# Kernel optimization log

Hardware: AMD Instinct MI355X
Metric: run time of the kernel (lower is better)

## Reference

```python
import jax, jax.numpy as jnp
import numpy as np

N, S, R, CM = 1, 128, 256, 256
C, CZ = 32, 128


def setup_inputs() -> dict:
    key = jax.random.key(0)
    k1, k2, k3, k4 = jax.random.split(key, 4)
    return {
        "msa_repr": jax.random.normal(k1, (N, S, R, CM), dtype=jnp.float32),
        "left_proj": jax.random.normal(k2, (CM, C), dtype=jnp.float32) * 0.05,
        "right_proj": jax.random.normal(k3, (CM, C), dtype=jnp.float32) * 0.05,
        "out_proj": jax.random.normal(k4, (C * C, CZ), dtype=jnp.float32) * 0.05,
    }


def reference(msa_repr, left_proj, right_proj, out_proj):
    # msa_repr: [N, S, R, CM]
    # Project to left/right activations and move R before S
    # (equivalent to torch matmul + transpose(-2, -3)).
    a = jnp.einsum("nsrm,mc->nrsc", msa_repr, left_proj)   # [N, R, S, C]
    b = jnp.einsum("nsrm,mc->nrsc", msa_repr, right_proj)  # [N, R, S, C]
    # Outer product contracted over the MSA dim S:
    # outer[n, r, t, c, e] = sum_s a[n, r, s, c] * b[n, t, s, e]
    outer = jnp.einsum("nrsc,ntse->nrtce", a, b)            # [N, R, R, C, C]
    n, r, t = outer.shape[:3]
    outer = outer.reshape(n, r, t, C * C)                   # [N, R, R, C*C]
    # Output projection to pair channels cz
    return outer @ out_proj                                 # [N, R, R, CZ]
```

## Files before the change

kernel.cpp:

```cpp
#include <hip/hip_runtime.h>

typedef __bf16 bf16x8 __attribute__((ext_vector_type(8)));
typedef __bf16 bf16x4 __attribute__((ext_vector_type(4)));
typedef float f32x16 __attribute__((ext_vector_type(16)));
typedef float f32x4 __attribute__((ext_vector_type(4)));

constexpr int S = 128, R = 256, CM = 256, C = 32, CZ = 128;

#define MFMA __builtin_amdgcn_mfma_f32_32x32x16_bf16

__device__ __forceinline__ bf16x4 cvt4(float a, float b, float c, float d) {
    bf16x4 r;
    r[0] = (__bf16)a; r[1] = (__bf16)b; r[2] = (__bf16)c; r[3] = (__bf16)d;
    return r;
}

__global__ __launch_bounds__(256) void k_wt(const float* __restrict__ W,
                                            __bf16* __restrict__ WTf) {
    int g = blockIdx.x * 256 + threadIdx.x;
    int cz = g & 127;
    int k = g >> 7;
    int e = k >> 5, c = k & 31;
    float v = W[(size_t)(c * 32 + e) * 128 + cz];
    WTf[((size_t)(k >> 3) * 128 + cz) * 8 + (k & 7)] = (__bf16)v;
}

__global__ __launch_bounds__(256) void k_wlr(const float* __restrict__ Lp,
                                             const float* __restrict__ Rp,
                                             __bf16* __restrict__ WLRT) {
    int c = blockIdx.x;
    int m = threadIdx.x;
    const float* src = (c < 32) ? Lp : Rp;
    WLRT[(size_t)c * 256 + m] = (__bf16)src[(size_t)m * 32 + (c & 31)];
}

__global__ __launch_bounds__(512) void k_proj(const float* __restrict__ msa,
                                              const __bf16* __restrict__ WLRT,
                                              __bf16* __restrict__ aTf,
                                              __bf16* __restrict__ bTf) {
    __shared__ __align__(16) __bf16 As[64 * 256];
    __shared__ __align__(16) char Pp[4 * 4096];
    const int r = blockIdx.x;
    const int sh = blockIdx.y;
    const int t = threadIdx.x;

#pragma unroll
    for (int it = 0; it < 8; ++it) {
        int idx = it * 512 + t;
        int row = idx >> 6;
        int cg = idx & 63;
        float4 v = *(const float4*)&msa[((size_t)(sh * 64 + row) * R + r) * CM + cg * 4];
        bf16x4 h = cvt4(v.x, v.y, v.z, v.w);
        int P = (cg >> 1) ^ (row & 15);
        *(bf16x4*)((char*)As + row * 512 + P * 16 + (cg & 1) * 8) = h;
    }
    __syncthreads();

    const int w = t >> 6;
    const int l = t & 63;
    const int l31 = t & 31;
    const int kh = (t >> 5) & 1;
    const int ksh = w >> 2;
    const int sd = (w >> 1) & 1;
    const int mi = w & 1;

    f32x16 acc;
#pragma unroll
    for (int q = 0; q < 16; ++q) acc[q] = 0.f;

    const bf16x8* wb = (const bf16x8*)&WLRT[(size_t)(sd * 32 + l31) * 256 + 8 * kh];
    const int srow = mi * 32 + l31;
    const char* arow = (const char*)As + srow * 512;

    __builtin_amdgcn_s_setprio(1);
#pragma unroll
    for (int j = 0; j < 8; ++j) {
        int ks = ksh * 8 + j;
        int P = (2 * ks + kh) ^ (srow & 15);
        bf16x8 af = *(const bf16x8*)(arow + P * 16);
        acc = MFMA(af, wb[2 * ks], acc, 0, 0, 0);
    }
    __builtin_amdgcn_s_setprio(0);

    char* pbase = Pp + (size_t)(sd * 2 + mi) * 4096;
    if (ksh == 1) {
#pragma unroll
        for (int pc = 0; pc < 4; ++pc) {
            f32x4 v;
            v[0] = acc[4 * pc + 0]; v[1] = acc[4 * pc + 1];
            v[2] = acc[4 * pc + 2]; v[3] = acc[4 * pc + 3];
            *(f32x4*)(pbase + ((pc * 64) + l) * 16) = v;
        }
    }
    __syncthreads();
    if (ksh == 0) {
#pragma unroll
        for (int pc = 0; pc < 4; ++pc) {
            f32x4 v = *(const f32x4*)(pbase + ((pc * 64) + l) * 16);
            acc[4 * pc + 0] += v[0]; acc[4 * pc + 1] += v[1];
            acc[4 * pc + 2] += v[2]; acc[4 * pc + 3] += v[3];
        }
        __bf16* dst = sd ? bTf : aTf;
        const int wg = sh * 2 + mi;
#pragma unroll
        for (int q = 0; q < 4; ++q) {
            size_t base = (size_t)r * 4096 + (size_t)(2 * wg + (q >> 1)) * 512 +
                          (size_t)(q & 1) * 256 + (size_t)l31 * 8 + 4 * kh;
            *(bf16x4*)&dst[base] = cvt4(acc[4 * q + 0], acc[4 * q + 1],
                                        acc[4 * q + 2], acc[4 * q + 3]);
        }
    }
}

__global__ __launch_bounds__(1024, 4) void k_main(const __bf16* __restrict__ aTf,
                                                  const __bf16* __restrict__ bTf,
                                                  const __bf16* __restrict__ WTf,
                                                  float* __restrict__ out) {
    __shared__ __align__(16) __bf16 Gs[64 * 1024];

    const int t = threadIdx.x;
    const int w = t >> 6;
    const int l = t & 63;
    const int lane = l & 31;
    const int kh = l >> 5;
    const int r0 = blockIdx.x * 8;
    const int t0 = blockIdx.y * 8;

    const int rg = w >> 2;
    const int tg = w & 3;

    f32x16 acc[2][2];
#pragma unroll
    for (int i = 0; i < 2; ++i)
#pragma unroll
        for (int j = 0; j < 2; ++j)
#pragma unroll
            for (int q = 0; q < 16; ++q) acc[i][j][q] = 0.f;

    const bf16x8* ap0 = (const bf16x8*)aTf + ((size_t)(r0 + 2 * rg + 0) * 512 + kh * 32 + lane);
    const bf16x8* ap1 = (const bf16x8*)aTf + ((size_t)(r0 + 2 * rg + 1) * 512 + kh * 32 + lane);
    const bf16x8* bp0 = (const bf16x8*)bTf + ((size_t)(t0 + 2 * tg + 0) * 512 + kh * 32 + lane);
    const bf16x8* bp1 = (const bf16x8*)bTf + ((size_t)(t0 + 2 * tg + 1) * 512 + kh * 32 + lane);

    bf16x8 A0[2], B0[2], A1[2], B1[2];
#define LDA(Aa, Bb, ks) do { \
    Aa[0] = ap0[(ks) * 64]; Aa[1] = ap1[(ks) * 64]; \
    Bb[0] = bp0[(ks) * 64]; Bb[1] = bp1[(ks) * 64]; } while (0)
#define PH_A(Aa, Bb) do { \
    __builtin_amdgcn_s_setprio(1); \
    acc[0][0] = MFMA(Aa[0], Bb[0], acc[0][0], 0, 0, 0); \
    acc[0][1] = MFMA(Aa[0], Bb[1], acc[0][1], 0, 0, 0); \
    acc[1][0] = MFMA(Aa[1], Bb[0], acc[1][0], 0, 0, 0); \
    acc[1][1] = MFMA(Aa[1], Bb[1], acc[1][1], 0, 0, 0); \
    __builtin_amdgcn_s_setprio(0); } while (0)

    LDA(A0, B0, 0);
#pragma unroll
    for (int ks = 0; ks < 8; ks += 2) {
        LDA(A1, B1, ks + 1);
        PH_A(A0, B0);
        LDA(A0, B0, (ks + 2) & 7);
        PH_A(A1, B1);
    }

#pragma unroll
    for (int i = 0; i < 2; ++i) {
#pragma unroll
        for (int j = 0; j < 2; ++j) {
            int p = (2 * rg + i) * 8 + 2 * tg + j;
            unsigned prow = (unsigned)p * 2048;
#pragma unroll
            for (int q = 0; q < 4; ++q) {
                int Lc = lane * 4 + q;
                int P = Lc ^ (p & 15) ^ (lane & 7);
                *(bf16x4*)((char*)Gs + prow + (unsigned)P * 16 + kh * 8) =
                    cvt4(acc[i][j][4 * q + 0], acc[i][j][4 * q + 1],
                         acc[i][j][4 * q + 2], acc[i][j][4 * q + 3]);
            }
        }
    }
    __syncthreads();

    const int kq = w >> 2;
    const int mt = (w >> 1) & 1;
    const int ng = w & 1;
    const int czl0 = ng * 64 + lane;
    const int czl1 = czl0 + 32;
    const bf16x8* wb0 = (const bf16x8*)WTf + ((size_t)kh * 128 + czl0);
    const bf16x8* wb1 = (const bf16x8*)WTf + ((size_t)kh * 128 + czl1);
    const unsigned prowG = (unsigned)(mt * 32 + lane) * 2048;
    const int p15 = lane & 15;

    f32x16 o0, o1;
#pragma unroll
    for (int q = 0; q < 16; ++q) { o0[q] = 0.f; o1[q] = 0.f; }

    bf16x8 Wa0, Wa1, Ga, Wb0_, Wb1_, Gb;
#define LDB(W0v, W1v, Gv, kk) do { \
    W0v = wb0[(size_t)(kk) * 256]; \
    W1v = wb1[(size_t)(kk) * 256]; \
    int Lr = (kk) * 2 + kh; \
    int P = Lr ^ p15 ^ ((Lr >> 2) & 7); \
    Gv = *(const bf16x8*)((const char*)Gs + prowG + (unsigned)P * 16); } while (0)
#define PHB(W0v, W1v, Gv) do { \
    __builtin_amdgcn_s_setprio(1); \
    o0 = MFMA(Gv, W0v, o0, 0, 0, 0); \
    o1 = MFMA(Gv, W1v, o1, 0, 0, 0); \
    __builtin_amdgcn_s_setprio(0); } while (0)

    LDB(Wa0, Wa1, Ga, kq * 16);
#pragma unroll
    for (int j = 0; j < 16; j += 2) {
        LDB(Wb0_, Wb1_, Gb, kq * 16 + ((j + 1) & 15));
        PHB(Wa0, Wa1, Ga);
        LDB(Wa0, Wa1, Ga, kq * 16 + ((j + 2) & 15));
        PHB(Wb0_, Wb1_, Gb);
    }
    __syncthreads();

    if (kq > 0) {
        char* pr = (char*)Gs + (size_t)((kq - 1) * 4 + mt * 2 + ng) * 8192;
#pragma unroll
        for (int oi = 0; oi < 2; ++oi) {
            const f32x16& ov = oi ? o1 : o0;
#pragma unroll
            for (int pc = 0; pc < 4; ++pc) {
                f32x4 v;
                v[0] = ov[4 * pc + 0]; v[1] = ov[4 * pc + 1];
                v[2] = ov[4 * pc + 2]; v[3] = ov[4 * pc + 3];
                *(f32x4*)(pr + ((oi * 4 + pc) * 64 + l) * 16) = v;
            }
        }
    }
    __syncthreads();

    if (kq == 0) {
#pragma unroll
        for (int kq2 = 1; kq2 < 4; ++kq2) {
            const char* pr = (const char*)Gs + (size_t)((kq2 - 1) * 4 + mt * 2 + ng) * 8192;
#pragma unroll
            for (int pc = 0; pc < 4; ++pc) {
                f32x4 v0 = *(const f32x4*)(pr + ((pc) * 64 + l) * 16);
                f32x4 v1 = *(const f32x4*)(pr + ((4 + pc) * 64 + l) * 16);
                o0[4 * pc + 0] += v0[0]; o0[4 * pc + 1] += v0[1];
                o0[4 * pc + 2] += v0[2]; o0[4 * pc + 3] += v0[3];
                o1[4 * pc + 0] += v1[0]; o1[4 * pc + 1] += v1[1];
                o1[4 * pc + 2] += v1[2]; o1[4 * pc + 3] += v1[3];
            }
        }
#pragma unroll
        for (int reg = 0; reg < 16; ++reg) {
            int pl = mt * 32 + (reg & 3) + 8 * (reg >> 2) + 4 * kh;
            int pr2 = pl >> 3, pt = pl & 7;
            out[((size_t)(r0 + pr2) * 256 + (t0 + pt)) * 128 + czl0] = o0[reg];
            out[((size_t)(r0 + pr2) * 256 + (t0 + pt)) * 128 + czl1] = o1[reg];
        }
    }
}

extern "C" void kernel_launch(void* const* d_in, const int* in_sizes, int n_in,
                              void* d_out, int out_size, void* d_ws, size_t ws_size,
                              hipStream_t stream) {
    const float* msa = (const float*)d_in[0];
    const float* left = (const float*)d_in[1];
    const float* right = (const float*)d_in[2];
    const float* W = (const float*)d_in[3];

    __bf16* aTf = (__bf16*)d_ws;
    __bf16* bTf = aTf + (size_t)R * 4096;
    __bf16* WTf = bTf + (size_t)R * 4096;
    __bf16* WLRT = WTf + (size_t)128 * 1024;
    float* outp = (float*)d_out;

    k_wt<<<512, 256, 0, stream>>>(W, WTf);
    k_wlr<<<64, 256, 0, stream>>>(left, right, WLRT);
    k_proj<<<dim3(256, 2), 512, 0, stream>>>(msa, WLRT, aTf, bTf);
    k_main<<<dim3(32, 32), 1024, 0, stream>>>(aTf, bTf, WTf, outp);
}
```

Before: 66.95 us.

## Stage a/b tiles in LDS, remap output-projection waves, merge prep kernels

The two weight-preparation kernels are merged into a single launch, removing one kernel launch. In k_main the block's 8 rows of a and 8 rows of b are first loaded cooperatively into LDS and then read from there for the outer-product MFMAs. Previously each wave fetched them from global memory directly, with redundant loads across waves. The output-projection stage is remapped so each wave loads one W fragment and reuses it for two G row tiles, halving W global loads per wave. The cost is an extra LDS staging pass and additional barriers.

```diff
diff --git a/kernel.cpp b/kernel.cpp
--- a/kernel.cpp
+++ b/kernel.cpp
@@ -15,23 +15,25 @@
     return r;
 }
 
-__global__ __launch_bounds__(256) void k_wt(const float* __restrict__ W,
-                                            __bf16* __restrict__ WTf) {
-    int g = blockIdx.x * 256 + threadIdx.x;
-    int cz = g & 127;
-    int k = g >> 7;
-    int e = k >> 5, c = k & 31;
-    float v = W[(size_t)(c * 32 + e) * 128 + cz];
-    WTf[((size_t)(k >> 3) * 128 + cz) * 8 + (k & 7)] = (__bf16)v;
-}
-
-__global__ __launch_bounds__(256) void k_wlr(const float* __restrict__ Lp,
-                                             const float* __restrict__ Rp,
-                                             __bf16* __restrict__ WLRT) {
-    int c = blockIdx.x;
-    int m = threadIdx.x;
-    const float* src = (c < 32) ? Lp : Rp;
-    WLRT[(size_t)c * 256 + m] = (__bf16)src[(size_t)m * 32 + (c & 31)];
+__global__ __launch_bounds__(256) void k_prep(const float* __restrict__ W,
+                                              const float* __restrict__ Lp,
+                                              const float* __restrict__ Rp,
+                                              __bf16* __restrict__ WTf,
+                                              __bf16* __restrict__ WLRT) {
+    int b = blockIdx.x;
+    if (b < 512) {
+        int g = b * 256 + threadIdx.x;
+        int cz = g & 127;
+        int k = g >> 7;
+        int e = k >> 5, c = k & 31;
+        float v = W[(size_t)(c * 32 + e) * 128 + cz];
+        WTf[((size_t)(k >> 3) * 128 + cz) * 8 + (k & 7)] = (__bf16)v;
+    } else {
+        int c = b - 512;
+        int m = threadIdx.x;
+        const float* src = (c < 32) ? Lp : Rp;
+        WLRT[(size_t)c * 256 + m] = (__bf16)src[(size_t)m * 32 + (c & 31)];
+    }
 }
 
 __global__ __launch_bounds__(512) void k_proj(const float* __restrict__ msa,
@@ -116,7 +118,7 @@
                                                   const __bf16* __restrict__ bTf,
                                                   const __bf16* __restrict__ WTf,
                                                   float* __restrict__ out) {
-    __shared__ __align__(16) __bf16 Gs[64 * 1024];
+    __shared__ __align__(16) __bf16 Lds[64 * 1024];
 
     const int t = threadIdx.x;
     const int w = t >> 6;
@@ -126,6 +128,26 @@
     const int r0 = blockIdx.x * 8;
     const int t0 = blockIdx.y * 8;
 
+    {
+        const bf16x8* ga = (const bf16x8*)(aTf + (size_t)r0 * 4096);
+        const bf16x8* gb = (const bf16x8*)(bTf + (size_t)t0 * 4096);
+        bf16x8* ls = (bf16x8*)Lds;
+        bf16x8 va[4], vb[4];
+#pragma unroll
+        for (int i = 0; i < 4; ++i) {
+            int idx = i * 1024 + t;
+            va[i] = ga[idx];
+            vb[i] = gb[idx];
+        }
+#pragma unroll
+        for (int i = 0; i < 4; ++i) {
+            int idx = i * 1024 + t;
+            ls[idx] = va[i];
+            ls[4096 + idx] = vb[i];
+        }
+    }
+    __syncthreads();
+
     const int rg = w >> 2;
     const int tg = w & 3;
 
@@ -137,15 +159,17 @@
 #pragma unroll
             for (int q = 0; q < 16; ++q) acc[i][j][q] = 0.f;
 
-    const bf16x8* ap0 = (const bf16x8*)aTf + ((size_t)(r0 + 2 * rg + 0) * 512 + kh * 32 + lane);
-    const bf16x8* ap1 = (const bf16x8*)aTf + ((size_t)(r0 + 2 * rg + 1) * 512 + kh * 32 + lane);
-    const bf16x8* bp0 = (const bf16x8*)bTf + ((size_t)(t0 + 2 * tg + 0) * 512 + kh * 32 + lane);
-    const bf16x8* bp1 = (const bf16x8*)bTf + ((size_t)(t0 + 2 * tg + 1) * 512 + kh * 32 + lane);
+    const char* a0p = (const char*)Lds + (2 * rg + 0) * 8192 + kh * 512 + lane * 16;
+    const char* a1p = (const char*)Lds + (2 * rg + 1) * 8192 + kh * 512 + lane * 16;
+    const char* b0p = (const char*)Lds + 65536 + (2 * tg + 0) * 8192 + kh * 512 + lane * 16;
+    const char* b1p = (const char*)Lds + 65536 + (2 * tg + 1) * 8192 + kh * 512 + lane * 16;
 
     bf16x8 A0[2], B0[2], A1[2], B1[2];
 #define LDA(Aa, Bb, ks) do { \
-    Aa[0] = ap0[(ks) * 64]; Aa[1] = ap1[(ks) * 64]; \
-    Bb[0] = bp0[(ks) * 64]; Bb[1] = bp1[(ks) * 64]; } while (0)
+    Aa[0] = *(const bf16x8*)(a0p + (ks) * 1024); \
+    Aa[1] = *(const bf16x8*)(a1p + (ks) * 1024); \
+    Bb[0] = *(const bf16x8*)(b0p + (ks) * 1024); \
+    Bb[1] = *(const bf16x8*)(b1p + (ks) * 1024); } while (0)
 #define PH_A(Aa, Bb) do { \
     __builtin_amdgcn_s_setprio(1); \
     acc[0][0] = MFMA(Aa[0], Bb[0], acc[0][0], 0, 0, 0); \
@@ -162,6 +186,7 @@
         LDA(A0, B0, (ks + 2) & 7);
         PH_A(A1, B1);
     }
+    __syncthreads();
 
 #pragma unroll
     for (int i = 0; i < 2; ++i) {
@@ -173,7 +198,7 @@
             for (int q = 0; q < 4; ++q) {
                 int Lc = lane * 4 + q;
                 int P = Lc ^ (p & 15) ^ (lane & 7);
-                *(bf16x4*)((char*)Gs + prow + (unsigned)P * 16 + kh * 8) =
+                *(bf16x4*)((char*)Lds + prow + (unsigned)P * 16 + kh * 8) =
                     cvt4(acc[i][j][4 * q + 0], acc[i][j][4 * q + 1],
                          acc[i][j][4 * q + 2], acc[i][j][4 * q + 3]);
             }
@@ -182,44 +207,42 @@
     __syncthreads();
 
     const int kq = w >> 2;
-    const int mt = (w >> 1) & 1;
-    const int ng = w & 1;
-    const int czl0 = ng * 64 + lane;
-    const int czl1 = czl0 + 32;
-    const bf16x8* wb0 = (const bf16x8*)WTf + ((size_t)kh * 128 + czl0);
-    const bf16x8* wb1 = (const bf16x8*)WTf + ((size_t)kh * 128 + czl1);
-    const unsigned prowG = (unsigned)(mt * 32 + lane) * 2048;
+    const int ns = w & 3;
+    const int czl = ns * 32 + lane;
+    const bf16x8* wb = (const bf16x8*)WTf + ((size_t)kh * 128 + czl);
+    const unsigned prow0 = (unsigned)lane * 2048;
+    const unsigned prow1 = (unsigned)(lane + 32) * 2048;
     const int p15 = lane & 15;
 
     f32x16 o0, o1;
 #pragma unroll
     for (int q = 0; q < 16; ++q) { o0[q] = 0.f; o1[q] = 0.f; }
 
-    bf16x8 Wa0, Wa1, Ga, Wb0_, Wb1_, Gb;
-#define LDB(W0v, W1v, Gv, kk) do { \
-    W0v = wb0[(size_t)(kk) * 256]; \
-    W1v = wb1[(size_t)(kk) * 256]; \
+    bf16x8 Wa, Ga0, Ga1, Wb_, Gb0, Gb1;
+#define LDB(Wv, G0v, G1v, kk) do { \
+    Wv = wb[(size_t)(kk) * 256]; \
     int Lr = (kk) * 2 + kh; \
     int P = Lr ^ p15 ^ ((Lr >> 2) & 7); \
-    Gv = *(const bf16x8*)((const char*)Gs + prowG + (unsigned)P * 16); } while (0)
-#define PHB(W0v, W1v, Gv) do { \
+    G0v = *(const bf16x8*)((const char*)Lds + prow0 + (unsigned)P * 16); \
+    G1v = *(const bf16x8*)((const char*)Lds + prow1 + (unsigned)P * 16); } while (0)
+#define PHB(Wv, G0v, G1v) do { \
     __builtin_amdgcn_s_setprio(1); \
-    o0 = MFMA(Gv, W0v, o0, 0, 0, 0); \
-    o1 = MFMA(Gv, W1v, o1, 0, 0, 0); \
+    o0 = MFMA(G0v, Wv, o0, 0, 0, 0); \
+    o1 = MFMA(G1v, Wv, o1, 0, 0, 0); \
     __builtin_amdgcn_s_setprio(0); } while (0)
 
-    LDB(Wa0, Wa1, Ga, kq * 16);
+    LDB(Wa, Ga0, Ga1, kq * 16);
 #pragma unroll
     for (int j = 0; j < 16; j += 2) {
-        LDB(Wb0_, Wb1_, Gb, kq * 16 + ((j + 1) & 15));
-        PHB(Wa0, Wa1, Ga);
-        LDB(Wa0, Wa1, Ga, kq * 16 + ((j + 2) & 15));
-        PHB(Wb0_, Wb1_, Gb);
+        LDB(Wb_, Gb0, Gb1, kq * 16 + ((j + 1) & 15));
+        PHB(Wa, Ga0, Ga1);
+        LDB(Wa, Ga0, Ga1, kq * 16 + ((j + 2) & 15));
+        PHB(Wb_, Gb0, Gb1);
     }
     __syncthreads();
 
     if (kq > 0) {
-        char* pr = (char*)Gs + (size_t)((kq - 1) * 4 + mt * 2 + ng) * 8192;
+        char* pr = (char*)Lds + (size_t)((kq - 1) * 4 + ns) * 8192;
 #pragma unroll
         for (int oi = 0; oi < 2; ++oi) {
             const f32x16& ov = oi ? o1 : o0;
@@ -237,7 +260,7 @@
     if (kq == 0) {
 #pragma unroll
         for (int kq2 = 1; kq2 < 4; ++kq2) {
-            const char* pr = (const char*)Gs + (size_t)((kq2 - 1) * 4 + mt * 2 + ng) * 8192;
+            const char* pr = (const char*)Lds + (size_t)((kq2 - 1) * 4 + ns) * 8192;
 #pragma unroll
             for (int pc = 0; pc < 4; ++pc) {
                 f32x4 v0 = *(const f32x4*)(pr + ((pc) * 64 + l) * 16);
@@ -250,10 +273,11 @@
         }
 #pragma unroll
         for (int reg = 0; reg < 16; ++reg) {
-            int pl = mt * 32 + (reg & 3) + 8 * (reg >> 2) + 4 * kh;
-            int pr2 = pl >> 3, pt = pl & 7;
-            out[((size_t)(r0 + pr2) * 256 + (t0 + pt)) * 128 + czl0] = o0[reg];
-            out[((size_t)(r0 + pr2) * 256 + (t0 + pt)) * 128 + czl1] = o1[reg];
+            int base = (reg & 3) + 8 * (reg >> 2) + 4 * kh;
+            int pl0 = base;
+            int pl1 = 32 + base;
+            out[((size_t)(r0 + (pl0 >> 3)) * 256 + (t0 + (pl0 & 7))) * 128 + czl] = o0[reg];
+            out[((size_t)(r0 + (pl1 >> 3)) * 256 + (t0 + (pl1 & 7))) * 128 + czl] = o1[reg];
         }
     }
 }
@@ -272,8 +296,7 @@
     __bf16* WLRT = WTf + (size_t)128 * 1024;
     float* outp = (float*)d_out;
 
-    k_wt<<<512, 256, 0, stream>>>(W, WTf);
-    k_wlr<<<64, 256, 0, stream>>>(left, right, WLRT);
+    k_prep<<<576, 256, 0, stream>>>(W, left, right, WTf, WLRT);
     k_proj<<<dim3(256, 2), 512, 0, stream>>>(msa, WLRT, aTf, bTf);
     k_main<<<dim3(32, 32), 1024, 0, stream>>>(aTf, bTf, WTf, outp);
 }
```

Result: faster. 64.16 us (-4.2%).

## Merge weight prep kernels and halve block sizes in projection and main kernels

Applied to the files above, without the earlier changes.

The two weight-conversion kernels are merged into one launch. The projection kernel now handles 32 MSA rows per 256-thread block instead of 64 rows per 512-thread block. The main kernel uses 512-thread blocks that each cover an 8x4 tile of (r,t) pairs instead of 8x8, which doubles the grid. The aim is to cut launch overhead and raise occupancy and the number of waves. The cost is more redundant loads of the aTf rows and the weights across blocks.

```diff
diff --git a/kernel.cpp b/kernel.cpp
--- a/kernel.cpp
+++ b/kernel.cpp
@@ -15,41 +15,43 @@
     return r;
 }
 
-__global__ __launch_bounds__(256) void k_wt(const float* __restrict__ W,
-                                            __bf16* __restrict__ WTf) {
-    int g = blockIdx.x * 256 + threadIdx.x;
-    int cz = g & 127;
-    int k = g >> 7;
-    int e = k >> 5, c = k & 31;
-    float v = W[(size_t)(c * 32 + e) * 128 + cz];
-    WTf[((size_t)(k >> 3) * 128 + cz) * 8 + (k & 7)] = (__bf16)v;
-}
-
-__global__ __launch_bounds__(256) void k_wlr(const float* __restrict__ Lp,
-                                             const float* __restrict__ Rp,
-                                             __bf16* __restrict__ WLRT) {
-    int c = blockIdx.x;
-    int m = threadIdx.x;
-    const float* src = (c < 32) ? Lp : Rp;
-    WLRT[(size_t)c * 256 + m] = (__bf16)src[(size_t)m * 32 + (c & 31)];
-}
-
-__global__ __launch_bounds__(512) void k_proj(const float* __restrict__ msa,
+__global__ __launch_bounds__(256) void k_prep(const float* __restrict__ W,
+                                              const float* __restrict__ Lp,
+                                              const float* __restrict__ Rp,
+                                              __bf16* __restrict__ WTf,
+                                              __bf16* __restrict__ WLRT) {
+    int b = blockIdx.x;
+    if (b < 512) {
+        int g = b * 256 + threadIdx.x;
+        int cz = g & 127;
+        int k = g >> 7;
+        int e = k >> 5, c = k & 31;
+        float v = W[(size_t)(c * 32 + e) * 128 + cz];
+        WTf[((size_t)(k >> 3) * 128 + cz) * 8 + (k & 7)] = (__bf16)v;
+    } else {
+        int c = b - 512;
+        int m = threadIdx.x;
+        const float* src = (c < 32) ? Lp : Rp;
+        WLRT[(size_t)c * 256 + m] = (__bf16)src[(size_t)m * 32 + (c & 31)];
+    }
+}
+
+__global__ __launch_bounds__(256) void k_proj(const float* __restrict__ msa,
                                               const __bf16* __restrict__ WLRT,
                                               __bf16* __restrict__ aTf,
                                               __bf16* __restrict__ bTf) {
-    __shared__ __align__(16) __bf16 As[64 * 256];
-    __shared__ __align__(16) char Pp[4 * 4096];
+    __shared__ __align__(16) __bf16 As[32 * 256];
+    __shared__ __align__(16) char Pp[2 * 4096];
     const int r = blockIdx.x;
-    const int sh = blockIdx.y;
+    const int sq = blockIdx.y;
     const int t = threadIdx.x;
 
 #pragma unroll
     for (int it = 0; it < 8; ++it) {
-        int idx = it * 512 + t;
+        int idx = it * 256 + t;
         int row = idx >> 6;
         int cg = idx & 63;
-        float4 v = *(const float4*)&msa[((size_t)(sh * 64 + row) * R + r) * CM + cg * 4];
+        float4 v = *(const float4*)&msa[((size_t)(sq * 32 + row) * R + r) * CM + cg * 4];
         bf16x4 h = cvt4(v.x, v.y, v.z, v.w);
         int P = (cg >> 1) ^ (row & 15);
         *(bf16x4*)((char*)As + row * 512 + P * 16 + (cg & 1) * 8) = h;
@@ -60,29 +62,27 @@
     const int l = t & 63;
     const int l31 = t & 31;
     const int kh = (t >> 5) & 1;
-    const int ksh = w >> 2;
-    const int sd = (w >> 1) & 1;
-    const int mi = w & 1;
+    const int sd = w & 1;
+    const int ksh = w >> 1;
 
     f32x16 acc;
 #pragma unroll
     for (int q = 0; q < 16; ++q) acc[q] = 0.f;
 
     const bf16x8* wb = (const bf16x8*)&WLRT[(size_t)(sd * 32 + l31) * 256 + 8 * kh];
-    const int srow = mi * 32 + l31;
-    const char* arow = (const char*)As + srow * 512;
+    const char* arow = (const char*)As + l31 * 512;
 
     __builtin_amdgcn_s_setprio(1);
 #pragma unroll
     for (int j = 0; j < 8; ++j) {
         int ks = ksh * 8 + j;
-        int P = (2 * ks + kh) ^ (srow & 15);
+        int P = (2 * ks + kh) ^ (l31 & 15);
         bf16x8 af = *(const bf16x8*)(arow + P * 16);
         acc = MFMA(af, wb[2 * ks], acc, 0, 0, 0);
     }
     __builtin_amdgcn_s_setprio(0);
 
-    char* pbase = Pp + (size_t)(sd * 2 + mi) * 4096;
+    char* pbase = Pp + (size_t)sd * 4096;
     if (ksh == 1) {
 #pragma unroll
         for (int pc = 0; pc < 4; ++pc) {
@@ -101,10 +101,9 @@
             acc[4 * pc + 2] += v[2]; acc[4 * pc + 3] += v[3];
         }
         __bf16* dst = sd ? bTf : aTf;
-        const int wg = sh * 2 + mi;
 #pragma unroll
         for (int q = 0; q < 4; ++q) {
-            size_t base = (size_t)r * 4096 + (size_t)(2 * wg + (q >> 1)) * 512 +
+            size_t base = (size_t)r * 4096 + (size_t)(2 * sq + (q >> 1)) * 512 +
                           (size_t)(q & 1) * 256 + (size_t)l31 * 8 + 4 * kh;
             *(bf16x4*)&dst[base] = cvt4(acc[4 * q + 0], acc[4 * q + 1],
                                         acc[4 * q + 2], acc[4 * q + 3]);
@@ -112,11 +111,11 @@
     }
 }
 
-__global__ __launch_bounds__(1024, 4) void k_main(const __bf16* __restrict__ aTf,
-                                                  const __bf16* __restrict__ bTf,
-                                                  const __bf16* __restrict__ WTf,
-                                                  float* __restrict__ out) {
-    __shared__ __align__(16) __bf16 Gs[64 * 1024];
+__global__ __launch_bounds__(512, 4) void k_main(const __bf16* __restrict__ aTf,
+                                                 const __bf16* __restrict__ bTf,
+                                                 const __bf16* __restrict__ WTf,
+                                                 float* __restrict__ out) {
+    __shared__ __align__(16) __bf16 Gs[32 * 1024];
 
     const int t = threadIdx.x;
     const int w = t >> 6;
@@ -124,10 +123,10 @@
     const int lane = l & 31;
     const int kh = l >> 5;
     const int r0 = blockIdx.x * 8;
-    const int t0 = blockIdx.y * 8;
-
-    const int rg = w >> 2;
-    const int tg = w & 3;
+    const int t0 = blockIdx.y * 4;
+
+    const int rg = w >> 1;
+    const int tg = w & 1;
 
     f32x16 acc[2][2];
 #pragma unroll
@@ -139,35 +138,33 @@
 
     const bf16x8* ap0 = (const bf16x8*)aTf + ((size_t)(r0 + 2 * rg + 0) * 512 + kh * 32 + lane);
     const bf16x8* ap1 = (const bf16x8*)aTf + ((size_t)(r0 + 2 * rg + 1) * 512 + kh * 32 + lane);
-    const bf16x8* bp0 = (const bf16x8*)bTf + ((size_t)(t0 + 2 * tg + 0) * 512 + kh * 32 + lane);
-    const bf16x8* bp1 = (const bf16x8*)bTf + ((size_t)(t0 + 2 * tg + 1) * 512 + kh * 32 + lane);
-
-    bf16x8 A0[2], B0[2], A1[2], B1[2];
-#define LDA(Aa, Bb, ks) do { \
-    Aa[0] = ap0[(ks) * 64]; Aa[1] = ap1[(ks) * 64]; \
-    Bb[0] = bp0[(ks) * 64]; Bb[1] = bp1[(ks) * 64]; } while (0)
-#define PH_A(Aa, Bb) do { \
+    const bf16x8* bq0 = (const bf16x8*)bTf + ((size_t)(t0 + 2 * tg + 0) * 512 + kh * 32 + lane);
+    const bf16x8* bq1 = (const bf16x8*)bTf + ((size_t)(t0 + 2 * tg + 1) * 512 + kh * 32 + lane);
+
+    bf16x8 Ap[2][2], Bp[2][2];
+#define LDA(s, ks) do { \
+    Ap[s][0] = ap0[(ks) * 64]; Ap[s][1] = ap1[(ks) * 64]; \
+    Bp[s][0] = bq0[(ks) * 64]; Bp[s][1] = bq1[(ks) * 64]; } while (0)
+#define PH_A(s) do { \
     __builtin_amdgcn_s_setprio(1); \
-    acc[0][0] = MFMA(Aa[0], Bb[0], acc[0][0], 0, 0, 0); \
-    acc[0][1] = MFMA(Aa[0], Bb[1], acc[0][1], 0, 0, 0); \
-    acc[1][0] = MFMA(Aa[1], Bb[0], acc[1][0], 0, 0, 0); \
-    acc[1][1] = MFMA(Aa[1], Bb[1], acc[1][1], 0, 0, 0); \
+    acc[0][0] = MFMA(Ap[s][0], Bp[s][0], acc[0][0], 0, 0, 0); \
+    acc[0][1] = MFMA(Ap[s][0], Bp[s][1], acc[0][1], 0, 0, 0); \
+    acc[1][0] = MFMA(Ap[s][1], Bp[s][0], acc[1][0], 0, 0, 0); \
+    acc[1][1] = MFMA(Ap[s][1], Bp[s][1], acc[1][1], 0, 0, 0); \
     __builtin_amdgcn_s_setprio(0); } while (0)
 
-    LDA(A0, B0, 0);
+    LDA(0, 0); LDA(1, 1);
 #pragma unroll
     for (int ks = 0; ks < 8; ks += 2) {
-        LDA(A1, B1, ks + 1);
-        PH_A(A0, B0);
-        LDA(A0, B0, (ks + 2) & 7);
-        PH_A(A1, B1);
+        PH_A(0); LDA(0, (ks + 2) & 7);
+        PH_A(1); LDA(1, (ks + 3) & 7);
     }
 
 #pragma unroll
     for (int i = 0; i < 2; ++i) {
 #pragma unroll
         for (int j = 0; j < 2; ++j) {
-            int p = (2 * rg + i) * 8 + 2 * tg + j;
+            int p = (2 * rg + i) * 4 + 2 * tg + j;
             unsigned prow = (unsigned)p * 2048;
 #pragma unroll
             for (int q = 0; q < 4; ++q) {
@@ -181,14 +178,13 @@
     }
     __syncthreads();
 
-    const int kq = w >> 2;
-    const int mt = (w >> 1) & 1;
+    const int kq = w >> 1;
     const int ng = w & 1;
     const int czl0 = ng * 64 + lane;
     const int czl1 = czl0 + 32;
     const bf16x8* wb0 = (const bf16x8*)WTf + ((size_t)kh * 128 + czl0);
     const bf16x8* wb1 = (const bf16x8*)WTf + ((size_t)kh * 128 + czl1);
-    const unsigned prowG = (unsigned)(mt * 32 + lane) * 2048;
+    const unsigned prowG = (unsigned)lane * 2048;
     const int p15 = lane & 15;
 
     f32x16 o0, o1;
@@ -219,7 +215,7 @@
     __syncthreads();
 
     if (kq > 0) {
-        char* pr = (char*)Gs + (size_t)((kq - 1) * 4 + mt * 2 + ng) * 8192;
+        char* pr = (char*)Gs + (size_t)((kq - 1) * 2 + ng) * 8192;
 #pragma unroll
         for (int oi = 0; oi < 2; ++oi) {
             const f32x16& ov = oi ? o1 : o0;
@@ -237,7 +233,7 @@
     if (kq == 0) {
 #pragma unroll
         for (int kq2 = 1; kq2 < 4; ++kq2) {
-            const char* pr = (const char*)Gs + (size_t)((kq2 - 1) * 4 + mt * 2 + ng) * 8192;
+            const char* pr = (const char*)Gs + (size_t)((kq2 - 1) * 2 + ng) * 8192;
 #pragma unroll
             for (int pc = 0; pc < 4; ++pc) {
                 f32x4 v0 = *(const f32x4*)(pr + ((pc) * 64 + l) * 16);
@@ -250,8 +246,8 @@
         }
 #pragma unroll
         for (int reg = 0; reg < 16; ++reg) {
-            int pl = mt * 32 + (reg & 3) + 8 * (reg >> 2) + 4 * kh;
-            int pr2 = pl >> 3, pt = pl & 7;
+            int pl = (reg & 3) + 8 * (reg >> 2) + 4 * kh;
+            int pr2 = pl >> 2, pt = pl & 3;
             out[((size_t)(r0 + pr2) * 256 + (t0 + pt)) * 128 + czl0] = o0[reg];
             out[((size_t)(r0 + pr2) * 256 + (t0 + pt)) * 128 + czl1] = o1[reg];
         }
@@ -272,8 +268,7 @@
     __bf16* WLRT = WTf + (size_t)128 * 1024;
     float* outp = (float*)d_out;
 
-    k_wt<<<512, 256, 0, stream>>>(W, WTf);
-    k_wlr<<<64, 256, 0, stream>>>(left, right, WLRT);
-    k_proj<<<dim3(256, 2), 512, 0, stream>>>(msa, WLRT, aTf, bTf);
-    k_main<<<dim3(32, 32), 1024, 0, stream>>>(aTf, bTf, WTf, outp);
-}
+    k_prep<<<576, 256, 0, stream>>>(W, left, right, WTf, WLRT);
+    k_proj<<<dim3(256, 4), 256, 0, stream>>>(msa, WLRT, aTf, bTf);
+    k_main<<<dim3(32, 64), 512, 0, stream>>>(aTf, bTf, WTf, outp);
+}
```

Measured after the change: 62.43 us. 6.8% less time.
